# Optimization experiments

Measured on AMD Instinct MI355X. Metric: run time of the kernel, lower is better.

Reference implementation:

```python
import jax, jax.numpy as jnp
import numpy as np

N_NODES = 50000
N_EDGES = 640000
N_GRAPHS = 256
H = 128
L = 4
X_DIM, P_DIM, E_DIM = 64, 16, 16


def setup_inputs() -> dict:
    key = jax.random.key(0)
    ks = jax.random.split(key, 16)
    s = 0.05
    inp = {
        "x": jax.random.normal(ks[0], (N_NODES, X_DIM), jnp.float32),
        "p": jax.random.normal(ks[1], (N_NODES, P_DIM), jnp.float32),
        "e_attr": jax.random.normal(ks[2], (N_EDGES, E_DIM), jnp.float32),
        "edge_index": jax.random.randint(ks[3], (2, N_EDGES), 0, N_NODES, jnp.int32),
        "batch": jnp.sort(jax.random.randint(ks[4], (N_NODES,), 0, N_GRAPHS, jnp.int32)),
        # embeddings
        "W_embed": jax.random.normal(ks[5], (X_DIM + P_DIM, H), jnp.float32) * s,
        "b_embed": jnp.zeros((H,), jnp.float32),
        "W_eembed": jax.random.normal(ks[6], (E_DIM, H), jnp.float32) * s,
        "b_eembed": jnp.zeros((H,), jnp.float32),
        # per-layer stacked params
        "Wm": jax.random.normal(ks[7], (L, 3 * H, H), jnp.float32) * s,
        "bm": jnp.zeros((L, H), jnp.float32),
        "Wh": jax.random.normal(ks[8], (L, 2 * H, H), jnp.float32) * s,
        "bh": jnp.zeros((L, H), jnp.float32),
        "We": jax.random.normal(ks[9], (L, 3 * H, H), jnp.float32) * s,
        "be": jnp.zeros((L, H), jnp.float32),
    }
    return inp


def reference(x, p, e_attr, W_embed, b_embed, W_eembed, b_eembed,
              Wm, bm, Wh, bh, We, be, edge_index, batch):
    # node embed: Linear(cat(x, p))
    h = jnp.concatenate([x, p], axis=1) @ W_embed + b_embed          # [N, H]
    e = e_attr @ W_eembed + b_eembed                                 # [E, H]
    send, rec = edge_index[0], edge_index[1]
    n_nodes = x.shape[0]
    for l in range(Wm.shape[0]):
        h_send, h_rec = h[send], h[rec]                              # gathers [E, H]
        cat_ser = jnp.concatenate([h_send, h_rec, e], axis=1)        # [E, 3H]
        messages = cat_ser @ Wm[l] + bm[l]                           # [E, H]
        messages_agg = jax.ops.segment_sum(messages, rec, num_segments=n_nodes)  # scatter_add
        h = jnp.concatenate([h, messages_agg], axis=1) @ Wh[l] + bh[l]
        # e_update uses h_send/h_rec gathered from the PRE-update h (as in torch code)
        e = cat_ser @ We[l] + be[l]
    # global_add_pool over graphs
    out = jax.ops.segment_sum(h, batch, num_segments=N_GRAPHS)       # [G, H]
    return out
```

## Files before the change

### kernel.cpp

```cpp
#include <hip/hip_runtime.h>
#include <cstdio>

#define NN 50000
#define NE 640000
#define NG 256
#define NL 4

#define SCAN_CHUNK 1024
#define NB_SCAN ((NN + SCAN_CHUNK - 1) / SCAN_CHUNK)

typedef unsigned short u16;
typedef unsigned int u32;
typedef __attribute__((ext_vector_type(8))) short short8v;
typedef __attribute__((ext_vector_type(4))) float f32x4;

static __device__ __forceinline__ float bf2f(u16 v) {
    return __uint_as_float(((u32)v) << 16);
}
static __device__ __forceinline__ u16 f2bf(float f) {
    u32 u = __float_as_uint(f);
    u += 0x7fff + ((u >> 16) & 1);
    return (u16)(u >> 16);
}

__global__ __launch_bounds__(256) void k_deg(
    const int* __restrict__ rec, int* __restrict__ deg)
{
    const int e = blockIdx.x * 256 + threadIdx.x;
    atomicAdd(&deg[rec[e]], 1);
}

__global__ __launch_bounds__(256) void k_prep_xp(
    const float* __restrict__ x, const float* __restrict__ p,
    u16* __restrict__ Axp)
{
    const int idx = blockIdx.x * 256 + threadIdx.x;
    const int row = idx / 48;
    const int c2 = idx - row * 48;
    const int c0 = c2 * 2;
    float f0, f1;
    if (c0 < 64)      { f0 = x[(size_t)row * 64 + c0]; f1 = x[(size_t)row * 64 + c0 + 1]; }
    else if (c0 < 80) { f0 = p[(size_t)row * 16 + c0 - 64]; f1 = p[(size_t)row * 16 + c0 - 63]; }
    else              { f0 = 0.f; f1 = 0.f; }
    ((u32*)Axp)[idx] = (u32)f2bf(f0) | ((u32)f2bf(f1) << 16);
}

__global__ __launch_bounds__(256) void k_wembed(
    const float* __restrict__ W, u16* __restrict__ Wp)
{
    const int idx = blockIdx.x * 256 + threadIdx.x;
    const int ks = idx >> 12;
    const int rem = idx & 4095;
    const int col = rem >> 5;
    const int kk = rem & 31;
    const int k = ks * 32 + kk;
    Wp[((size_t)ks * 128 + col) * 32 + kk] = f2bf(k < 80 ? W[k * 128 + col] : 0.f);
}

__global__ __launch_bounds__(256) void k_embed(
    const u16* __restrict__ Axp, const u16* __restrict__ Wp,
    const float* __restrict__ b, u16* __restrict__ h)
{
    const int t = threadIdx.x;
    const int lane = t & 63;
    const int w = t >> 6;
    const int rb = blockIdx.x * 128 + w * 32;
    const int l15 = lane & 15;
    const int kg  = lane >> 4;

    int r0 = rb + l15;      if (r0 > NN - 1) r0 = NN - 1;
    int r1 = rb + 16 + l15; if (r1 > NN - 1) r1 = NN - 1;

    f32x4 acc[2][8];
    #pragma unroll
    for (int m = 0; m < 2; ++m)
        #pragma unroll
        for (int n = 0; n < 8; ++n) acc[m][n] = (f32x4){0.f, 0.f, 0.f, 0.f};

    #pragma unroll
    for (int ks = 0; ks < 3; ++ks) {
        const short8v a0 = *(const short8v*)(Axp + (size_t)r0 * 96 + ks * 32 + kg * 8);
        const short8v a1 = *(const short8v*)(Axp + (size_t)r1 * 96 + ks * 32 + kg * 8);
        const u16* bb = Wp + ((size_t)ks * 128 + l15) * 32 + kg * 8;
        #pragma unroll
        for (int nf = 0; nf < 8; ++nf) {
            const short8v bv = *(const short8v*)(bb + (size_t)nf * 16 * 32);
            acc[0][nf] = __builtin_amdgcn_mfma_f32_16x16x32_bf16(a0, bv, acc[0][nf], 0, 0, 0);
            acc[1][nf] = __builtin_amdgcn_mfma_f32_16x16x32_bf16(a1, bv, acc[1][nf], 0, 0, 0);
        }
    }

    #pragma unroll
    for (int m = 0; m < 2; ++m) {
        #pragma unroll
        for (int r = 0; r < 4; ++r) {
            const int row = rb + m * 16 + kg * 4 + r;
            if (row < NN) {
                #pragma unroll
                for (int nf = 0; nf < 8; ++nf) {
                    const int col = nf * 16 + l15;
                    h[(size_t)row * 128 + col] = f2bf(acc[m][nf][r] + b[col]);
                }
            }
        }
    }
}

__global__ __launch_bounds__(256) void k_wprep(
    const float* __restrict__ Wm, const float* __restrict__ Wh,
    const float* __restrict__ We, const float* __restrict__ bm,
    float* __restrict__ Wb, float* __restrict__ cvec)
{
    const int idx = blockIdx.x * 256 + threadIdx.x;
    const int total = 4 * 512 * 256;
    if (idx < total) {
        const int l = idx >> 17;
        const int rem = idx & 131071;
        const int k = rem >> 8;
        const int c = rem & 255;
        const float* Wm_l = Wm + (size_t)l * 384 * 128;
        const float* Wh_l = Wh + (size_t)l * 256 * 128;
        const float* We_l = We + (size_t)l * 384 * 128;
        float v;
        if (k < 128) {
            v = (c < 128) ? Wh_l[k * 128 + c] : 0.f;
        } else {
            const int kk  = (k - 128) & 127;
            const int blk = (k - 128) >> 7;
            const int roff = (blk == 0) ? 128 : (blk == 1) ? 0 : 256;
            if (c < 128) {
                float s = 0.f;
                #pragma unroll 4
                for (int j = 0; j < 128; ++j)
                    s += Wm_l[(roff + kk) * 128 + j] * Wh_l[(128 + j) * 128 + c];
                v = s;
            } else {
                v = We_l[(roff + kk) * 128 + (c - 128)];
            }
        }
        Wb[idx] = v;
    } else if (idx < total + 512) {
        const int r = idx - total;
        const int l = r >> 7;
        const int c = r & 127;
        const float* Wh_l = Wh + (size_t)l * 256 * 128;
        const float* bm_l = bm + l * 128;
        float s = 0.f;
        #pragma unroll 4
        for (int j = 0; j < 128; ++j) s += bm_l[j] * Wh_l[(128 + j) * 128 + c];
        cvec[r] = s;
    }
}

__global__ __launch_bounds__(256) void k_wswz(
    const float* __restrict__ Wb, u16* __restrict__ Bp)
{
    const int idx = blockIdx.x * 256 + threadIdx.x;
    const int l = idx >> 17;
    const int rem = idx & 131071;
    const int k = rem >> 8;
    const int n = rem & 255;
    Bp[(((size_t)l * 16 + (k >> 5)) * 256 + n) * 32 + (k & 31)] = f2bf(Wb[idx]);
}

__global__ __launch_bounds__(256) void k_scanA(
    const int* __restrict__ deg, int* __restrict__ part)
{
    __shared__ int red[256];
    const int t = threadIdx.x;
    const int base = blockIdx.x * SCAN_CHUNK + t * 4;
    int s = 0;
    #pragma unroll
    for (int i = 0; i < 4; ++i) {
        const int idx = base + i;
        if (idx < NN) s += deg[idx];
    }
    red[t] = s;
    __syncthreads();
    for (int off = 128; off > 0; off >>= 1) {
        if (t < off) red[t] += red[t + off];
        __syncthreads();
    }
    if (t == 0) part[blockIdx.x] = red[0];
}

__global__ __launch_bounds__(64) void k_scanB(int* part)
{
    if (threadIdx.x == 0) {
        int run = 0;
        for (int b = 0; b < NB_SCAN; ++b) {
            const int v = part[b];
            part[b] = run;
            run += v;
        }
    }
}

__global__ __launch_bounds__(256) void k_scanC(
    const int* __restrict__ deg, const int* __restrict__ part,
    int* __restrict__ offs, int* __restrict__ cursor)
{
    __shared__ int ts[256];
    const int t = threadIdx.x;
    const int base = blockIdx.x * SCAN_CHUNK + t * 4;
    int v[4]; int s = 0;
    #pragma unroll
    for (int i = 0; i < 4; ++i) {
        const int idx = base + i;
        v[i] = (idx < NN) ? deg[idx] : 0;
        s += v[i];
    }
    ts[t] = s;
    __syncthreads();
    for (int off = 1; off < 256; off <<= 1) {
        int val = ts[t];
        if (t >= off) val += ts[t - off];
        __syncthreads();
        ts[t] = val;
        __syncthreads();
    }
    int run = part[blockIdx.x] + ((t == 0) ? 0 : ts[t - 1]);
    #pragma unroll
    for (int i = 0; i < 4; ++i) {
        const int idx = base + i;
        if (idx < NN) { offs[idx] = run; cursor[idx] = run; run += v[i]; }
    }
}

__global__ __launch_bounds__(256) void k_fill(
    const int* __restrict__ send, const int* __restrict__ rec,
    int* __restrict__ cursor, int* __restrict__ csr, int* __restrict__ csr_e)
{
    const int e = blockIdx.x * 256 + threadIdx.x;
    const int r = rec[e];
    const int pos = atomicAdd(&cursor[r], 1);
    csr[pos] = send[e];
    csr_e[pos] = e;
}

__global__ __launch_bounds__(256) void k_sea_se0(
    const float* __restrict__ ea, const int* __restrict__ csr_e,
    const int* __restrict__ offs, const int* __restrict__ deg,
    const float* __restrict__ Wee, const float* __restrict__ bee,
    u16* __restrict__ Se)
{
    __shared__ float sea[4][16];
    const int t = threadIdx.x;
    const int lane = t & 63;
    const int w = t >> 6;
    const int nb = blockIdx.x * 4;
    const int node = nb + w;
    const int g = lane >> 4;
    const int l16 = lane & 15;
    const int off = offs[node];
    const int d = deg[node];

    float acc = 0.f;
    for (int j = g; j < d; j += 4) {
        const int eid = csr_e[off + j];
        acc += ea[(size_t)eid * 16 + l16];
    }
    acc += __shfl_xor(acc, 16);
    acc += __shfl_xor(acc, 32);
    if (g == 0) sea[w][l16] = acc;
    __syncthreads();

    const int c = t & 127;
    #pragma unroll
    for (int q = 0; q < 2; ++q) {
        const int n = (t >> 7) + 2 * q;
        const int nd = nb + n;
        float a = (float)deg[nd] * bee[c];
        #pragma unroll
        for (int k = 0; k < 16; ++k) a += sea[n][k] * Wee[k * 128 + c];
        Se[(size_t)nd * 128 + c] = f2bf(a);
    }
}

__global__ __launch_bounds__(256) void k_gather(
    const u16* __restrict__ h, const int* __restrict__ csr,
    const int* __restrict__ offs, const int* __restrict__ deg,
    u16* __restrict__ Sh)
{
    const int t = threadIdx.x;
    const int lane = t & 63;
    const int node = blockIdx.x * 4 + (t >> 6);
    const int g = lane >> 4;
    const int l16 = lane & 15;
    const int off = offs[node];
    const int d = deg[node];
    const uint4* hp = (const uint4*)h;

    float a[8], b[8];
    #pragma unroll
    for (int i = 0; i < 8; ++i) { a[i] = 0.f; b[i] = 0.f; }

    int j = g;
    for (; j + 4 < d; j += 8) {
        const int s0 = csr[off + j];
        const int s1 = csr[off + j + 4];
        const uint4 v0 = hp[(size_t)s0 * 16 + l16];
        const uint4 v1 = hp[(size_t)s1 * 16 + l16];
        a[0] += bf2f((u16)(v0.x & 0xffff)); a[1] += bf2f((u16)(v0.x >> 16));
        a[2] += bf2f((u16)(v0.y & 0xffff)); a[3] += bf2f((u16)(v0.y >> 16));
        a[4] += bf2f((u16)(v0.z & 0xffff)); a[5] += bf2f((u16)(v0.z >> 16));
        a[6] += bf2f((u16)(v0.w & 0xffff)); a[7] += bf2f((u16)(v0.w >> 16));
        b[0] += bf2f((u16)(v1.x & 0xffff)); b[1] += bf2f((u16)(v1.x >> 16));
        b[2] += bf2f((u16)(v1.y & 0xffff)); b[3] += bf2f((u16)(v1.y >> 16));
        b[4] += bf2f((u16)(v1.z & 0xffff)); b[5] += bf2f((u16)(v1.z >> 16));
        b[6] += bf2f((u16)(v1.w & 0xffff)); b[7] += bf2f((u16)(v1.w >> 16));
    }
    if (j < d) {
        const uint4 v0 = hp[(size_t)csr[off + j] * 16 + l16];
        a[0] += bf2f((u16)(v0.x & 0xffff)); a[1] += bf2f((u16)(v0.x >> 16));
        a[2] += bf2f((u16)(v0.y & 0xffff)); a[3] += bf2f((u16)(v0.y >> 16));
        a[4] += bf2f((u16)(v0.z & 0xffff)); a[5] += bf2f((u16)(v0.z >> 16));
        a[6] += bf2f((u16)(v0.w & 0xffff)); a[7] += bf2f((u16)(v0.w >> 16));
    }
    #pragma unroll
    for (int i = 0; i < 8; ++i) {
        float s = a[i] + b[i];
        s += __shfl_xor(s, 16);
        s += __shfl_xor(s, 32);
        a[i] = s;
    }
    if (g == 0) {
        uint4 o;
        o.x = (u32)f2bf(a[0]) | ((u32)f2bf(a[1]) << 16);
        o.y = (u32)f2bf(a[2]) | ((u32)f2bf(a[3]) << 16);
        o.z = (u32)f2bf(a[4]) | ((u32)f2bf(a[5]) << 16);
        o.w = (u32)f2bf(a[6]) | ((u32)f2bf(a[7]) << 16);
        ((uint4*)Sh)[(size_t)node * 16 + l16] = o;
    }
}

template<bool FULL>
__global__ __launch_bounds__(256) void k_dense(
    const u16* __restrict__ h, const u16* __restrict__ Sh,
    const u16* __restrict__ Se, const int* __restrict__ deg,
    const u16* __restrict__ Bp, const float* __restrict__ cvec,
    const float* __restrict__ bh, const float* __restrict__ be,
    u16* __restrict__ h_out, u16* __restrict__ Se_out)
{
    const int t = threadIdx.x;
    const int lane = t & 63;
    const int w = t >> 6;
    if (!FULL && w >= 2) return;
    const int cb = w * 64;
    const int rb = blockIdx.x * 32;
    const int l15 = lane & 15;
    const int kg  = lane >> 4;

    int r0 = rb + l15;      if (r0 > NN - 1) r0 = NN - 1;
    int r1 = rb + 16 + l15; if (r1 > NN - 1) r1 = NN - 1;

    short8v Ah[2][4], As[2][4], Ae[2][4];
    #pragma unroll
    for (int k4 = 0; k4 < 4; ++k4) {
        const int ko = k4 * 32 + kg * 8;
        Ah[0][k4] = *(const short8v*)(h  + (size_t)r0 * 128 + ko);
        Ah[1][k4] = *(const short8v*)(h  + (size_t)r1 * 128 + ko);
        As[0][k4] = *(const short8v*)(Sh + (size_t)r0 * 128 + ko);
        As[1][k4] = *(const short8v*)(Sh + (size_t)r1 * 128 + ko);
        Ae[0][k4] = *(const short8v*)(Se + (size_t)r0 * 128 + ko);
        Ae[1][k4] = *(const short8v*)(Se + (size_t)r1 * 128 + ko);
    }

    f32x4 accP[2][4], accQ[2][4];
    #pragma unroll
    for (int m = 0; m < 2; ++m)
        #pragma unroll
        for (int n = 0; n < 4; ++n) {
            accP[m][n] = (f32x4){0.f, 0.f, 0.f, 0.f};
            accQ[m][n] = (f32x4){0.f, 0.f, 0.f, 0.f};
        }

    #pragma unroll
    for (int s = 0; s < 4; ++s) {
        #pragma unroll
        for (int k4 = 0; k4 < 4; ++k4) {
            const int ks = s * 4 + k4;
            const u16* bb = Bp + (((size_t)ks * 256) + cb + l15) * 32 + kg * 8;
            #pragma unroll
            for (int nf = 0; nf < 4; ++nf) {
                const short8v b = *(const short8v*)(bb + (size_t)nf * 16 * 32);
                if (s == 0) {
                    accP[0][nf] = __builtin_amdgcn_mfma_f32_16x16x32_bf16(Ah[0][k4], b, accP[0][nf], 0, 0, 0);
                    accP[1][nf] = __builtin_amdgcn_mfma_f32_16x16x32_bf16(Ah[1][k4], b, accP[1][nf], 0, 0, 0);
                } else if (s == 1) {
                    accQ[0][nf] = __builtin_amdgcn_mfma_f32_16x16x32_bf16(Ah[0][k4], b, accQ[0][nf], 0, 0, 0);
                    accQ[1][nf] = __builtin_amdgcn_mfma_f32_16x16x32_bf16(Ah[1][k4], b, accQ[1][nf], 0, 0, 0);
                } else if (s == 2) {
                    accP[0][nf] = __builtin_amdgcn_mfma_f32_16x16x32_bf16(As[0][k4], b, accP[0][nf], 0, 0, 0);
                    accP[1][nf] = __builtin_amdgcn_mfma_f32_16x16x32_bf16(As[1][k4], b, accP[1][nf], 0, 0, 0);
                } else {
                    accP[0][nf] = __builtin_amdgcn_mfma_f32_16x16x32_bf16(Ae[0][k4], b, accP[0][nf], 0, 0, 0);
                    accP[1][nf] = __builtin_amdgcn_mfma_f32_16x16x32_bf16(Ae[1][k4], b, accP[1][nf], 0, 0, 0);
                }
            }
        }
    }

    #pragma unroll
    for (int m = 0; m < 2; ++m) {
        #pragma unroll
        for (int r = 0; r < 4; ++r) {
            const int row = rb + m * 16 + kg * 4 + r;
            if (row < NN) {
                const float dg = (float)deg[row];
                if (cb < 128) {
                    #pragma unroll
                    for (int nf = 0; nf < 4; ++nf) {
                        const int col = cb + nf * 16 + l15;
                        h_out[(size_t)row * 128 + col] =
                            f2bf(accP[m][nf][r] + dg * accQ[m][nf][r] + bh[col] + dg * cvec[col]);
                    }
                } else {
                    #pragma unroll
                    for (int nf = 0; nf < 4; ++nf) {
                        const int col = cb - 128 + nf * 16 + l15;
                        Se_out[(size_t)row * 128 + col] =
                            f2bf(accP[m][nf][r] + dg * accQ[m][nf][r] + dg * be[col]);
                    }
                }
            }
        }
    }
}

__global__ __launch_bounds__(256) void k_pool(
    const u16* __restrict__ h, const int* __restrict__ batch,
    float* __restrict__ out)
{
    const int t = threadIdx.x;
    const int col = t & 127;
    const int half = t >> 7;
    const int base = blockIdx.x * 64 + half * 32;
    float acc = 0.f;
    int curg = -1;
    for (int i = 0; i < 32; ++i) {
        const int n = base + i;
        if (n >= NN) break;
        const int g = batch[n];
        if (g != curg) {
            if (curg >= 0) atomicAdd(&out[curg * 128 + col], acc);
            curg = g; acc = 0.f;
        }
        acc += bf2f(h[(size_t)n * 128 + col]);
    }
    if (curg >= 0) atomicAdd(&out[curg * 128 + col], acc);
}

extern "C" void kernel_launch(void* const* d_in, const int* in_sizes, int n_in,
                              void* d_out, int out_size, void* d_ws, size_t ws_size,
                              hipStream_t stream)
{
    const float* x       = (const float*)d_in[0];
    const float* p       = (const float*)d_in[1];
    const float* ea      = (const float*)d_in[2];
    const int*   eidx    = (const int*)d_in[3];
    const int*   batch   = (const int*)d_in[4];
    const float* W_embed = (const float*)d_in[5];
    const float* b_embed = (const float*)d_in[6];
    const float* W_ee    = (const float*)d_in[7];
    const float* b_ee    = (const float*)d_in[8];
    const float* Wm      = (const float*)d_in[9];
    const float* bm      = (const float*)d_in[10];
    const float* Wh      = (const float*)d_in[11];
    const float* bh      = (const float*)d_in[12];
    const float* We      = (const float*)d_in[13];
    const float* be      = (const float*)d_in[14];
    const int* send = eidx;
    const int* rec  = eidx + NE;

    char* w = (char*)d_ws;
    const size_t NHb = (size_t)NN * 128 * sizeof(u16);
    u16* hA  = (u16*)w; w += NHb;
    u16* hB  = (u16*)w; w += NHb;
    u16* SeA = (u16*)w; w += NHb;
    u16* SeB = (u16*)w; w += NHb;
    u16* Sh  = (u16*)w; w += NHb;
    u16* Axp = (u16*)w;  w += (size_t)NN * 96 * 2;
    int*  deg    = (int*)w;   w += (size_t)NN * 4;
    int*  offs   = (int*)w;   w += (size_t)(NN + 4) * 4;
    int*  cursor = (int*)w;   w += (size_t)NN * 4;
    int*  csr    = (int*)w;   w += (size_t)NE * 4;
    int*  csr_e  = (int*)w;   w += (size_t)NE * 4;
    int*  part   = (int*)w;   w += 64 * 4;
    float* Wb    = (float*)w; w += (size_t)4 * 512 * 256 * 4;
    float* cvec  = (float*)w; w += 512 * 4;
    u16*  Bp     = (u16*)w;   w += (size_t)4 * 512 * 256 * 2;
    u16*  Wpe    = (u16*)w;   w += (size_t)3 * 128 * 32 * 2;
    const size_t need = (size_t)(w - (char*)d_ws);
    if (ws_size < need) {
        fprintf(stderr, "[kernel_launch] ws_size=%zu < needed=%zu — skipping\n",
                ws_size, need);
        return;
    }

    float* out = (float*)d_out;

    hipMemsetAsync(d_out, 0, (size_t)NG * 128 * sizeof(float), stream);
    hipMemsetAsync(deg, 0, (size_t)NN * sizeof(int), stream);

    k_deg<<<NE / 256, 256, 0, stream>>>(rec, deg);
    k_prep_xp<<<NN * 48 / 256, 256, 0, stream>>>(x, p, Axp);
    k_wembed<<<3 * 128 * 32 / 256, 256, 0, stream>>>(W_embed, Wpe);
    k_embed<<<(NN + 127) / 128, 256, 0, stream>>>(Axp, Wpe, b_embed, hA);
    k_wprep<<<(4 * 512 * 256 + 512 + 255) / 256, 256, 0, stream>>>(Wm, Wh, We, bm, Wb, cvec);
    k_wswz<<<4 * 512 * 256 / 256, 256, 0, stream>>>(Wb, Bp);
    k_scanA<<<NB_SCAN, 256, 0, stream>>>(deg, part);
    k_scanB<<<1, 64, 0, stream>>>(part);
    k_scanC<<<NB_SCAN, 256, 0, stream>>>(deg, part, offs, cursor);
    k_fill<<<NE / 256, 256, 0, stream>>>(send, rec, cursor, csr, csr_e);
    k_sea_se0<<<NN / 4, 256, 0, stream>>>(ea, csr_e, offs, deg, W_ee, b_ee, SeA);

    u16* h_cur = hA;   u16* h_nxt = hB;
    u16* Se_cur = SeA; u16* Se_nxt = SeB;
    for (int l = 0; l < NL; ++l) {
        k_gather<<<NN / 4, 256, 0, stream>>>(h_cur, csr, offs, deg, Sh);
        if (l < NL - 1)
            k_dense<true><<<(NN + 31) / 32, 256, 0, stream>>>(h_cur, Sh, Se_cur,
                deg, Bp + (size_t)l * 512 * 256,
                cvec + l * 128, bh + l * 128, be + l * 128, h_nxt, Se_nxt);
        else
            k_dense<false><<<(NN + 31) / 32, 256, 0, stream>>>(h_cur, Sh, Se_cur,
                deg, Bp + (size_t)l * 512 * 256,
                cvec + l * 128, bh + l * 128, be + l * 128, h_nxt, Se_nxt);
        u16* tmp;
        tmp = h_cur;  h_cur  = h_nxt;  h_nxt  = tmp;
        tmp = Se_cur; Se_cur = Se_nxt; Se_nxt = tmp;
    }
    k_pool<<<(NN + 63) / 64, 256, 0, stream>>>(h_cur, batch, out);
}
```

Baseline: 510.1 us.

## Stage dense-layer weights through double-buffered LDS with async global-to-LDS loads

The dense kernel now copies each 32-wide K slice of the swizzled weight matrix into a double-buffered shared-memory tile using global_load_lds, instead of every wave reading B fragments straight from global memory. The weight layout is re-swizzled to match this staging pattern, and A-operand loads are spread across the K loop rather than all preloaded, which lowers register pressure. In exchange the kernel takes a __syncthreads per K step and 32KB of LDS per block, and in the non-FULL variant idle waves must stay alive to help with staging.

```diff
diff --git a/kernel.cpp b/kernel.cpp
--- a/kernel.cpp
+++ b/kernel.cpp
@@ -21,6 +21,11 @@
     u32 u = __float_as_uint(f);
     u += 0x7fff + ((u >> 16) & 1);
     return (u16)(u >> 16);
+}
+static __device__ __forceinline__ void gload_lds16(const u16* g, u16* l) {
+    __builtin_amdgcn_global_load_lds(
+        (const __attribute__((address_space(1))) u32*)g,
+        (__attribute__((address_space(3))) u32*)l, 16, 0, 0);
 }
 
 __global__ __launch_bounds__(256) void k_deg(
@@ -160,7 +165,10 @@
     const int rem = idx & 131071;
     const int k = rem >> 8;
     const int n = rem & 255;
-    Bp[(((size_t)l * 16 + (k >> 5)) * 256 + n) * 32 + (k & 31)] = f2bf(Wb[idx]);
+    const int ks = k >> 5;
+    const int kg = (k >> 3) & 3;
+    const int kk = k & 7;
+    Bp[(size_t)l * 131072 + (((size_t)ks * 4 + kg) * 256 + n) * 8 + kk] = f2bf(Wb[idx]);
 }
 
 __global__ __launch_bounds__(256) void k_scanA(
@@ -342,10 +350,10 @@
     const float* __restrict__ bh, const float* __restrict__ be,
     u16* __restrict__ h_out, u16* __restrict__ Se_out)
 {
+    __shared__ u16 Bs[2][8192];
     const int t = threadIdx.x;
     const int lane = t & 63;
     const int w = t >> 6;
-    if (!FULL && w >= 2) return;
     const int cb = w * 64;
     const int rb = blockIdx.x * 32;
     const int l15 = lane & 15;
@@ -354,18 +362,17 @@
     int r0 = rb + l15;      if (r0 > NN - 1) r0 = NN - 1;
     int r1 = rb + 16 + l15; if (r1 > NN - 1) r1 = NN - 1;
 
-    short8v Ah[2][4], As[2][4], Ae[2][4];
-    #pragma unroll
-    for (int k4 = 0; k4 < 4; ++k4) {
-        const int ko = k4 * 32 + kg * 8;
-        Ah[0][k4] = *(const short8v*)(h  + (size_t)r0 * 128 + ko);
-        Ah[1][k4] = *(const short8v*)(h  + (size_t)r1 * 128 + ko);
-        As[0][k4] = *(const short8v*)(Sh + (size_t)r0 * 128 + ko);
-        As[1][k4] = *(const short8v*)(Sh + (size_t)r1 * 128 + ko);
-        Ae[0][k4] = *(const short8v*)(Se + (size_t)r0 * 128 + ko);
-        Ae[1][k4] = *(const short8v*)(Se + (size_t)r1 * 128 + ko);
-    }
-
+    #define STAGE(buf, ks)                                                  \
+        {                                                                   \
+            const u16* src = Bp + (size_t)(ks) * 8192 + t * 8;              \
+            u16* dst = &Bs[buf][t * 8];                                     \
+            gload_lds16(src,        dst);                                   \
+            gload_lds16(src + 2048, dst + 2048);                            \
+            gload_lds16(src + 4096, dst + 4096);                            \
+            gload_lds16(src + 6144, dst + 6144);                            \
+        }
+
+    short8v Ah[2][4];
     f32x4 accP[2][4], accQ[2][4];
     #pragma unroll
     for (int m = 0; m < 2; ++m)
@@ -375,31 +382,52 @@
             accQ[m][n] = (f32x4){0.f, 0.f, 0.f, 0.f};
         }
 
-    #pragma unroll
-    for (int s = 0; s < 4; ++s) {
-        #pragma unroll
-        for (int k4 = 0; k4 < 4; ++k4) {
-            const int ks = s * 4 + k4;
-            const u16* bb = Bp + (((size_t)ks * 256) + cb + l15) * 32 + kg * 8;
+    STAGE(0, 0)
+    __syncthreads();
+
+    #pragma unroll
+    for (int ks = 0; ks < 16; ++ks) {
+        const int cur = ks & 1;
+        if (ks < 15) STAGE(cur ^ 1, ks + 1)
+
+        const int s = ks >> 2;
+        const int k4 = ks & 3;
+        const int ko = k4 * 32 + kg * 8;
+
+        if (FULL || w < 2) {
+            short8v a0, a1;
+            if (s == 0) {
+                a0 = *(const short8v*)(h + (size_t)r0 * 128 + ko);
+                a1 = *(const short8v*)(h + (size_t)r1 * 128 + ko);
+                Ah[0][k4] = a0; Ah[1][k4] = a1;
+            } else if (s == 1) {
+                a0 = Ah[0][k4]; a1 = Ah[1][k4];
+            } else if (s == 2) {
+                a0 = *(const short8v*)(Sh + (size_t)r0 * 128 + ko);
+                a1 = *(const short8v*)(Sh + (size_t)r1 * 128 + ko);
+            } else {
+                a0 = *(const short8v*)(Se + (size_t)r0 * 128 + ko);
+                a1 = *(const short8v*)(Se + (size_t)r1 * 128 + ko);
+            }
+
+            const u16* bs = &Bs[cur][((size_t)kg * 256 + cb + l15) * 8];
             #pragma unroll
             for (int nf = 0; nf < 4; ++nf) {
-                const short8v b = *(const short8v*)(bb + (size_t)nf * 16 * 32);
-                if (s == 0) {
-                    accP[0][nf] = __builtin_amdgcn_mfma_f32_16x16x32_bf16(Ah[0][k4], b, accP[0][nf], 0, 0, 0);
-                    accP[1][nf] = __builtin_amdgcn_mfma_f32_16x16x32_bf16(Ah[1][k4], b, accP[1][nf], 0, 0, 0);
-                } else if (s == 1) {
-                    accQ[0][nf] = __builtin_amdgcn_mfma_f32_16x16x32_bf16(Ah[0][k4], b, accQ[0][nf], 0, 0, 0);
-                    accQ[1][nf] = __builtin_amdgcn_mfma_f32_16x16x32_bf16(Ah[1][k4], b, accQ[1][nf], 0, 0, 0);
-                } else if (s == 2) {
-                    accP[0][nf] = __builtin_amdgcn_mfma_f32_16x16x32_bf16(As[0][k4], b, accP[0][nf], 0, 0, 0);
-                    accP[1][nf] = __builtin_amdgcn_mfma_f32_16x16x32_bf16(As[1][k4], b, accP[1][nf], 0, 0, 0);
+                const short8v b = *(const short8v*)(bs + nf * 128);
+                if (s == 1) {
+                    accQ[0][nf] = __builtin_amdgcn_mfma_f32_16x16x32_bf16(a0, b, accQ[0][nf], 0, 0, 0);
+                    accQ[1][nf] = __builtin_amdgcn_mfma_f32_16x16x32_bf16(a1, b, accQ[1][nf], 0, 0, 0);
                 } else {
-                    accP[0][nf] = __builtin_amdgcn_mfma_f32_16x16x32_bf16(Ae[0][k4], b, accP[0][nf], 0, 0, 0);
-                    accP[1][nf] = __builtin_amdgcn_mfma_f32_16x16x32_bf16(Ae[1][k4], b, accP[1][nf], 0, 0, 0);
+                    accP[0][nf] = __builtin_amdgcn_mfma_f32_16x16x32_bf16(a0, b, accP[0][nf], 0, 0, 0);
+                    accP[1][nf] = __builtin_amdgcn_mfma_f32_16x16x32_bf16(a1, b, accP[1][nf], 0, 0, 0);
                 }
             }
         }
-    }
+        __syncthreads();
+    }
+    #undef STAGE
+
+    if (!FULL && w >= 2) return;
 
     #pragma unroll
     for (int m = 0; m < 2; ++m) {
@@ -521,11 +549,11 @@
         k_gather<<<NN / 4, 256, 0, stream>>>(h_cur, csr, offs, deg, Sh);
         if (l < NL - 1)
             k_dense<true><<<(NN + 31) / 32, 256, 0, stream>>>(h_cur, Sh, Se_cur,
-                deg, Bp + (size_t)l * 512 * 256,
+                deg, Bp + (size_t)l * 131072,
                 cvec + l * 128, bh + l * 128, be + l * 128, h_nxt, Se_nxt);
         else
             k_dense<false><<<(NN + 31) / 32, 256, 0, stream>>>(h_cur, Sh, Se_cur,
-                deg, Bp + (size_t)l * 512 * 256,
+                deg, Bp + (size_t)l * 131072,
                 cvec + l * 128, bh + l * 128, be + l * 128, h_nxt, Se_nxt);
         u16* tmp;
         tmp = h_cur;  h_cur  = h_nxt;  h_nxt  = tmp;
```

Result: faster. 458.3 us (-10.2%).
